# Kernel tuning notes

Hardware: AMD Instinct MI355X
Metric: run time of the kernel (lower is better)

## Reference

```python
import jax, jax.numpy as jnp
import numpy as np

IN, H, B = 1024, 1024, 8192


def _uniform(key, shape, stdv):
    return jax.random.uniform(key, shape, jnp.float32, -stdv, stdv)


def setup_inputs() -> dict:
    key = jax.random.key(0)
    ks = jax.random.split(key, 20)
    stdv = 1.0 / np.sqrt(H)
    inp = {
        "x": jax.random.normal(ks[0], (B, IN), jnp.float32),
        "h": jax.random.normal(ks[1], (B, H), jnp.float32),
        "c": jax.random.normal(ks[2], (B, H), jnp.float32),
        # fused input->gates weight [IN, 4H] (gate order: I, F, G, O) and bias [4H]
        "Wi": _uniform(ks[3], (IN, 4 * H), stdv),
        "bi": _uniform(ks[4], (4 * H,), stdv),
        # fused hidden->gates weight [H, 4H] and bias [4H]
        "Wh": _uniform(ks[5], (H, 4 * H), stdv),
        "bh": _uniform(ks[6], (4 * H,), stdv),
    }
    return inp


def reference(x, h, c, Wi, bi, Wh, bh):
    # Two fused GEMMs replacing the 8 separate nn.Linear calls (same math).
    gates = x @ Wi + bi + h @ Wh + bh  # [B, 4H]
    gI, gF, gG, gO = jnp.split(gates, 4, axis=-1)
    I = jax.nn.sigmoid(gI)
    F = jax.nn.sigmoid(gF)
    G = jnp.tanh(gG)   # nlF = Tanh
    O = jax.nn.sigmoid(gO)
    c_ = F * c + I * G
    h_ = O * jnp.tanh(c_)  # nlF2 = Tanh
    return (h_, c_)
```

## Files before the change

kernel.cpp:

```cpp
#include <hip/hip_runtime.h>
#include <stdint.h>

#define IN_DIM 1024
#define H_DIM  1024
#define BATCH  8192
#define KDIM   2048
#define NDIM   4096
#define BM     256
#define BN     256
#define BK     64
#define NT     (KDIM / BK)

typedef __bf16 bf16x8 __attribute__((ext_vector_type(8)));
typedef float  f32x4  __attribute__((ext_vector_type(4)));
typedef unsigned int u32;

static __device__ __forceinline__ unsigned short f2bf(float f) {
  u32 u = __builtin_bit_cast(u32, f);
  u += 0x7FFFu + ((u >> 16) & 1u);
  return (unsigned short)(u >> 16);
}

static __device__ __forceinline__ float sigm(float x) {
  return 1.0f / (1.0f + __expf(-x));
}
static __device__ __forceinline__ float tanh_fast(float x) {
  float e = __expf(-2.0f * fabsf(x));
  float t = (1.0f - e) / (1.0f + e);
  return copysignf(t, x);
}

__global__ void prep_all(const float* __restrict__ x, const float* __restrict__ h,
                         const float* __restrict__ Wi, const float* __restrict__ Wh,
                         const float* __restrict__ bi, const float* __restrict__ bh,
                         unsigned short* __restrict__ A,
                         unsigned short* __restrict__ Bt,
                         float* __restrict__ bias) {
  __shared__ float tile[32][33];
  const int b = blockIdx.x;
  const int t = threadIdx.x;

  if (b < 2048) {
    const int total = BATCH * KDIM / 4;
    for (int i = b * 256 + t; i < total; i += 2048 * 256) {
      int bb = i >> 9;
      int k = (i & 511) << 2;
      const float* src = (k < IN_DIM) ? (x + (size_t)bb * IN_DIM + k)
                                      : (h + (size_t)bb * H_DIM + (k - IN_DIM));
      float4 v = *reinterpret_cast<const float4*>(src);
      ushort4 o;
      o.x = f2bf(v.x); o.y = f2bf(v.y); o.z = f2bf(v.z); o.w = f2bf(v.w);
      *reinterpret_cast<ushort4*>(A + (size_t)bb * KDIM + k) = o;
    }
  } else if (b < 10240) {
    int bb = b - 2048;
    int k0 = (bb & 63) * 32;
    int c0 = (bb >> 6) * 32;
    int tx = t & 31;
    int ty = t >> 5;
    const float* src = (k0 < IN_DIM) ? (Wi + (size_t)k0 * NDIM)
                                     : (Wh + (size_t)(k0 - IN_DIM) * NDIM);
    for (int i = 0; i < 4; i++) {
      int r = ty + 8 * i;
      tile[r][tx] = src[(size_t)r * NDIM + c0 + tx];
    }
    __syncthreads();
    int g = c0 >> 10;
    int ubase = c0 & 1023;
    for (int i = 0; i < 4; i++) {
      int cc = ty + 8 * i;
      int u = ubase + cc;
      int j = ((u >> 4) << 6) + (g << 4) + (u & 15);
      Bt[(size_t)j * KDIM + k0 + tx] = f2bf(tile[tx][cc]);
    }
  } else {
    int j = (b - 10240) * 256 + t;
    int u = ((j >> 6) << 4) + (j & 15);
    int g = (j >> 4) & 3;
    int c = (g << 10) + u;
    bias[j] = bi[c] + bh[c];
  }
}

static __device__ __forceinline__ void gload_lds16(const void* g, void* l) {
  __builtin_amdgcn_global_load_lds(
      (const __attribute__((address_space(1))) u32*)g,
      (__attribute__((address_space(3))) u32*)l, 16, 0, 0);
}

#define MFMA __builtin_amdgcn_mfma_f32_16x16x32_bf16
#define SGB  __builtin_amdgcn_sched_group_barrier

__launch_bounds__(512, 2)
__global__ void lstm_gemm(const unsigned short* __restrict__ A,
                          const unsigned short* __restrict__ Bt,
                          const float* __restrict__ bias,
                          const float* __restrict__ Cin,
                          float* __restrict__ Hout,
                          float* __restrict__ Cout) {
  __shared__ __align__(16) char smem[131072];

  const int t  = threadIdx.x;
  const int l  = t & 63;
  const int w  = t >> 6;
  const int lane16 = l & 15;
  const int kg = l >> 4;
  const int wr = w >> 2;
  const int wc = w & 3;

  int bid = blockIdx.x;
  int swz = (bid & 7) * 64 + (bid >> 3);
  int brow = (swz >> 4) * BM;
  int bcol = (swz & 15) * BN;

  int slot0 = w * 128 + l, slot1 = slot0 + 64;
  int rih0 = slot0 >> 3, rih1 = slot1 >> 3;
  int c0 = (slot0 & 7) ^ (rih0 & 7), c1 = (slot1 & 7) ^ (rih1 & 7);

  const unsigned short* a0q0 = A + (size_t)(brow + (rih0 >> 6) * 128 + (rih0 & 63)) * KDIM + c0 * 8;
  const unsigned short* a0q1 = A + (size_t)(brow + (rih1 >> 6) * 128 + (rih1 & 63)) * KDIM + c1 * 8;
  const unsigned short* a1q0 = a0q0 + 131072;
  const unsigned short* a1q1 = a0q1 + 131072;
  const unsigned short* b0q0 = Bt + (size_t)(bcol + (rih0 >> 5) * 64 + (rih0 & 31)) * KDIM + c0 * 8;
  const unsigned short* b0q1 = Bt + (size_t)(bcol + (rih1 >> 5) * 64 + (rih1 & 31)) * KDIM + c1 * 8;
  const unsigned short* b1q0 = b0q0 + 65536;
  const unsigned short* b1q1 = b0q1 + 65536;

#define GL(gp, loff) gload_lds16((gp), smem + (loff) + w * 2048 + l * 16)

  const int msk = (lane16 & 7) << 4;
  char* vA0 = smem + wr * 8192 + lane16 * 128 + ((kg * 16) ^ msk);
  char* vA1 = smem + wr * 8192 + lane16 * 128 + ((64 + kg * 16) ^ msk);
  char* vB0 = smem + 65536 + wc * 4096 + lane16 * 128 + ((kg * 16) ^ msk);
  char* vB1 = smem + 65536 + wc * 4096 + lane16 * 128 + ((64 + kg * 16) ^ msk);

  f32x4 acc[8][4];
#pragma unroll
  for (int m = 0; m < 8; m++)
#pragma unroll
    for (int n = 0; n < 4; n++) acc[m][n] = (f32x4){0.f, 0.f, 0.f, 0.f};

  GL(a0q0, 0);                 GL(a0q1, 1024);
  GL(b0q0, 65536);             GL(b0q1, 65536 + 1024);
  GL(a1q0, 16384);             GL(a1q1, 16384 + 1024);
  GL(b1q0, 65536 + 16384);     GL(b1q1, 65536 + 16384 + 1024);
  GL(a0q0 + 64, 32768);        GL(a0q1 + 64, 32768 + 1024);
  GL(b0q0 + 64, 65536 + 32768);GL(b0q1 + 64, 65536 + 32768 + 1024);
  asm volatile("s_waitcnt vmcnt(4)" ::: "memory");
  __builtin_amdgcn_s_barrier();
  __builtin_amdgcn_sched_barrier(0);
  GL(a1q0 + 64, 32768 + 16384); GL(a1q1 + 64, 32768 + 16384 + 1024);

  bf16x8 afrA[4][2], afrB[4][2], bfr[4][2];

#pragma unroll
  for (int mm = 0; mm < 4; mm++) {
    afrA[mm][0] = *(const bf16x8*)(vA0 + mm * 2048);
    afrA[mm][1] = *(const bf16x8*)(vA1 + mm * 2048);
  }
#pragma unroll
  for (int nn = 0; nn < 2; nn++) {
    bfr[nn][0] = *(const bf16x8*)(vB0 + nn * 2048);
    bfr[nn][1] = *(const bf16x8*)(vB1 + nn * 2048);
  }
  a0q0 += 128; a0q1 += 128; a1q0 += 128; a1q1 += 128;
  b0q0 += 128; b0q1 += 128; b1q0 += 64;  b1q1 += 64;

#define BODY(P)                                                              \
  {                                                                          \
    \
    GL(b1q0, 65536 + ((P)^1)*32768 + 16384);                                 \
    GL(b1q1, 65536 + ((P)^1)*32768 + 16384 + 1024);                          \
                           \
    __builtin_amdgcn_s_setprio(1);                                           \
    _Pragma("unroll") for (int nn = 2; nn < 4; nn++) {                       \
      bfr[nn][0] = *(const bf16x8*)(vB0 + (P)*32768 + 16384 + (nn-2)*2048);  \
      bfr[nn][1] = *(const bf16x8*)(vB1 + (P)*32768 + 16384 + (nn-2)*2048);  \
    }                                                                        \
    _Pragma("unroll") for (int mm = 0; mm < 4; mm++)                         \
      _Pragma("unroll") for (int nn = 0; nn < 2; nn++) {                     \
        acc[mm][nn] = MFMA(afrA[mm][0], bfr[nn][0], acc[mm][nn], 0, 0, 0);   \
        acc[mm][nn] = MFMA(afrA[mm][1], bfr[nn][1], acc[mm][nn], 0, 0, 0);   \
      }                                                                      \
    SGB(0x100, 1, 0); SGB(0x8, 4, 0);                                        \
    SGB(0x100, 1, 0); SGB(0x8, 4, 0);                                        \
    SGB(0x100, 1, 0); SGB(0x8, 4, 0);                                        \
    SGB(0x100, 1, 0); SGB(0x8, 4, 0);                                        \
    __builtin_amdgcn_s_setprio(0);                                           \
    __builtin_amdgcn_s_barrier();                                 \
    __builtin_amdgcn_sched_barrier(0);                                       \
         \
    GL(a0q0, (P)*32768);                                                     \
    GL(a0q1, (P)*32768 + 1024);                                              \
                       \
    __builtin_amdgcn_s_setprio(1);                                           \
    _Pragma("unroll") for (int mm = 0; mm < 4; mm++) {                       \
      afrB[mm][0] = *(const bf16x8*)(vA0 + (P)*32768 + 16384 + mm*2048);     \
      afrB[mm][1] = *(const bf16x8*)(vA1 + (P)*32768 + 16384 + mm*2048);     \
    }                                                                        \
    _Pragma("unroll") for (int mm = 0; mm < 4; mm++)                         \
      _Pragma("unroll") for (int nn = 2; nn < 4; nn++) {                     \
        acc[mm][nn] = MFMA(afrA[mm][0], bfr[nn][0], acc[mm][nn], 0, 0, 0);   \
        acc[mm][nn] = MFMA(afrA[mm][1], bfr[nn][1], acc[mm][nn], 0, 0, 0);   \
      }                                                                      \
    SGB(0x100, 2, 0); SGB(0x8, 4, 0);                                        \
    SGB(0x100, 2, 0); SGB(0x8, 4, 0);                                        \
    SGB(0x100, 2, 0); SGB(0x8, 4, 0);                                        \
    SGB(0x100, 2, 0); SGB(0x8, 4, 0);                                        \
    __builtin_amdgcn_s_setprio(0);                                           \
        \
    GL(b0q0, 65536 + (P)*32768);                                             \
    GL(b0q1, 65536 + (P)*32768 + 1024);                                      \
                            \
    __builtin_amdgcn_s_setprio(1);                                           \
    _Pragma("unroll") for (int mm = 0; mm < 4; mm++)                         \
      _Pragma("unroll") for (int nn = 0; nn < 2; nn++) {                     \
        acc[4+mm][nn] = MFMA(afrB[mm][0], bfr[nn][0], acc[4+mm][nn], 0, 0, 0);\
        acc[4+mm][nn] = MFMA(afrB[mm][1], bfr[nn][1], acc[4+mm][nn], 0, 0, 0);\
      }                                                                      \
    __builtin_amdgcn_s_setprio(0);                                           \
    \
    asm volatile("s_waitcnt vmcnt(4)" ::: "memory");                         \
    __builtin_amdgcn_s_barrier();                                 \
    __builtin_amdgcn_sched_barrier(0);                                       \
           \
    GL(a1q0, (P)*32768 + 16384);                                             \
    GL(a1q1, (P)*32768 + 16384 + 1024);                                      \
             \
    __builtin_amdgcn_s_setprio(1);                                           \
    _Pragma("unroll") for (int mm = 0; mm < 4; mm++) {                       \
      afrA[mm][0] = *(const bf16x8*)(vA0 + ((P)^1)*32768 + mm*2048);         \
      afrA[mm][1] = *(const bf16x8*)(vA1 + ((P)^1)*32768 + mm*2048);         \
    }                                                                        \
    _Pragma("unroll") for (int nn = 0; nn < 2; nn++) {                       \
      bfr[nn][0] = *(const bf16x8*)(vB0 + ((P)^1)*32768 + nn*2048);          \
      bfr[nn][1] = *(const bf16x8*)(vB1 + ((P)^1)*32768 + nn*2048);          \
    }                                                                        \
    _Pragma("unroll") for (int mm = 0; mm < 4; mm++)                         \
      _Pragma("unroll") for (int nn = 2; nn < 4; nn++) {                     \
        acc[4+mm][nn] = MFMA(afrB[mm][0], bfr[nn][0], acc[4+mm][nn], 0, 0, 0);\
        acc[4+mm][nn] = MFMA(afrB[mm][1], bfr[nn][1], acc[4+mm][nn], 0, 0, 0);\
      }                                                                      \
    SGB(0x100, 3, 0); SGB(0x8, 4, 0);                                        \
    SGB(0x100, 3, 0); SGB(0x8, 4, 0);                                        \
    SGB(0x100, 3, 0); SGB(0x8, 4, 0);                                        \
    SGB(0x100, 3, 0); SGB(0x8, 4, 0);                                        \
    __builtin_amdgcn_s_setprio(0);                                           \
    a0q0 += 64; a0q1 += 64; a1q0 += 64; a1q1 += 64;                          \
    b0q0 += 64; b0q1 += 64; b1q0 += 64; b1q1 += 64;                          \
  }

  for (int it = 0; it < NT / 2; ++it) {
    BODY(0)
    BODY(1)
  }
#undef BODY
#undef GL

  asm volatile("s_waitcnt vmcnt(0)" ::: "memory");

  const int U = (bcol >> 2) + wc * 16 + lane16;
  const float* cinp = Cin + (size_t)(brow + wr * 128 + kg * 4) * H_DIM + U;
  float cin[32];
#pragma unroll
  for (int m = 0; m < 8; m++)
#pragma unroll
    for (int r = 0; r < 4; r++)
      cin[m * 4 + r] = cinp[(size_t)(m * 16 + r) * H_DIM];
  float bv[4];
#pragma unroll
  for (int nn = 0; nn < 4; nn++)
    bv[nn] = bias[bcol + wc * 64 + nn * 16 + lane16];

  float* hp = Hout + (size_t)(brow + wr * 128 + kg * 4) * H_DIM + U;
  float* cp = Cout + (size_t)(brow + wr * 128 + kg * 4) * H_DIM + U;
#pragma unroll
  for (int m = 0; m < 8; m++)
#pragma unroll
    for (int r = 0; r < 4; r++) {
      float Ig = sigm(acc[m][0][r] + bv[0]);
      float Fg = sigm(acc[m][1][r] + bv[1]);
      float Gg = tanh_fast(acc[m][2][r] + bv[2]);
      float Og = sigm(acc[m][3][r] + bv[3]);
      float cn = Fg * cin[m * 4 + r] + Ig * Gg;
      size_t off = (size_t)(m * 16 + r) * H_DIM;
      hp[off] = Og * tanh_fast(cn);
      cp[off] = cn;
    }
}

extern "C" void kernel_launch(void* const* d_in, const int* in_sizes, int n_in,
                              void* d_out, int out_size, void* d_ws, size_t ws_size,
                              hipStream_t stream) {
  const float* x  = (const float*)d_in[0];
  const float* h  = (const float*)d_in[1];
  const float* c  = (const float*)d_in[2];
  const float* Wi = (const float*)d_in[3];
  const float* bi = (const float*)d_in[4];
  const float* Wh = (const float*)d_in[5];
  const float* bh = (const float*)d_in[6];

  float* out  = (float*)d_out;
  float* Hout = out;
  float* Cout = out + (size_t)BATCH * H_DIM;

  unsigned short* Abf = (unsigned short*)d_ws;
  unsigned short* Btb = (unsigned short*)((char*)d_ws + 33554432);
  float*          bsf = (float*)((char*)d_ws + 50331648);

  prep_all<<<10256, 256, 0, stream>>>(x, h, Wi, Wh, bi, bh, Abf, Btb, bsf);
  lstm_gemm<<<512, 512, 0, stream>>>(Abf, Btb, bsf, c, Hout, Cout);
}
```

Baseline: 152.1 us.

## Shrink GEMM block tile to 128x256 with BK=32 and 4-wave blocks

```diff
diff --git a/kernel.cpp b/kernel.cpp
--- a/kernel.cpp
+++ b/kernel.cpp
@@ -6,9 +6,9 @@
 #define BATCH  8192
 #define KDIM   2048
 #define NDIM   4096
-#define BM     256
+#define BM     128
 #define BN     256
-#define BK     64
+#define BK     32
 #define NT     (KDIM / BK)
 
 typedef __bf16 bf16x8 __attribute__((ext_vector_type(8)));
@@ -91,48 +91,43 @@
 #define MFMA __builtin_amdgcn_mfma_f32_16x16x32_bf16
 #define SGB  __builtin_amdgcn_sched_group_barrier
 
-__launch_bounds__(512, 2)
+__launch_bounds__(256, 2)
 __global__ void lstm_gemm(const unsigned short* __restrict__ A,
                           const unsigned short* __restrict__ Bt,
                           const float* __restrict__ bias,
                           const float* __restrict__ Cin,
                           float* __restrict__ Hout,
                           float* __restrict__ Cout) {
-  __shared__ __align__(16) char smem[131072];
+  __shared__ __align__(16) char smem[49152];
 
   const int t  = threadIdx.x;
   const int l  = t & 63;
   const int w  = t >> 6;
   const int lane16 = l & 15;
   const int kg = l >> 4;
-  const int wr = w >> 2;
-  const int wc = w & 3;
+  const int wc = w;
 
   int bid = blockIdx.x;
-  int swz = (bid & 7) * 64 + (bid >> 3);
-  int brow = (swz >> 4) * BM;
-  int bcol = (swz & 15) * BN;
-
-  int slot0 = w * 128 + l, slot1 = slot0 + 64;
-  int rih0 = slot0 >> 3, rih1 = slot1 >> 3;
-  int c0 = (slot0 & 7) ^ (rih0 & 7), c1 = (slot1 & 7) ^ (rih1 & 7);
-
-  const unsigned short* a0q0 = A + (size_t)(brow + (rih0 >> 6) * 128 + (rih0 & 63)) * KDIM + c0 * 8;
-  const unsigned short* a0q1 = A + (size_t)(brow + (rih1 >> 6) * 128 + (rih1 & 63)) * KDIM + c1 * 8;
-  const unsigned short* a1q0 = a0q0 + 131072;
-  const unsigned short* a1q1 = a0q1 + 131072;
-  const unsigned short* b0q0 = Bt + (size_t)(bcol + (rih0 >> 5) * 64 + (rih0 & 31)) * KDIM + c0 * 8;
-  const unsigned short* b0q1 = Bt + (size_t)(bcol + (rih1 >> 5) * 64 + (rih1 & 31)) * KDIM + c1 * 8;
-  const unsigned short* b1q0 = b0q0 + 65536;
-  const unsigned short* b1q1 = b0q1 + 65536;
-
-#define GL(gp, loff) gload_lds16((gp), smem + (loff) + w * 2048 + l * 16)
-
-  const int msk = (lane16 & 7) << 4;
-  char* vA0 = smem + wr * 8192 + lane16 * 128 + ((kg * 16) ^ msk);
-  char* vA1 = smem + wr * 8192 + lane16 * 128 + ((64 + kg * 16) ^ msk);
-  char* vB0 = smem + 65536 + wc * 4096 + lane16 * 128 + ((kg * 16) ^ msk);
-  char* vB1 = smem + 65536 + wc * 4096 + lane16 * 128 + ((64 + kg * 16) ^ msk);
+  int swz = (bid & 7) * 128 + (bid >> 3);
+  int tile_m = swz >> 4;
+  int tile_n = swz & 15;
+  int brow = tile_m * BM;
+  int bRowB = tile_n * BN;
+
+  const int cth = (l & 3) ^ ((l >> 3) & 3);
+  const int srow = w * 16 + (l >> 2);
+  const unsigned short* aq0 = A + (size_t)(brow + srow) * KDIM + cth * 8;
+  const unsigned short* aq1 = aq0 + (size_t)64 * KDIM;
+  const unsigned short* bq0 = Bt + (size_t)(bRowB + srow) * KDIM + cth * 8;
+  const unsigned short* bq1 = bq0 + (size_t)64 * KDIM;
+  const unsigned short* bq2 = bq0 + (size_t)128 * KDIM;
+  const unsigned short* bq3 = bq0 + (size_t)192 * KDIM;
+
+#define GL(gp, loff) gload_lds16((gp), smem + (loff) + w * 1024 + l * 16)
+
+  const int rsw = ((kg ^ ((lane16 >> 1) & 3)) << 4);
+  char* vRA = smem + lane16 * 64 + rsw;
+  char* vRB = smem + 16384 + wc * 4096 + lane16 * 64 + rsw;
 
   f32x4 acc[8][4];
 #pragma unroll
@@ -140,114 +135,82 @@
 #pragma unroll
     for (int n = 0; n < 4; n++) acc[m][n] = (f32x4){0.f, 0.f, 0.f, 0.f};
 
-  GL(a0q0, 0);                 GL(a0q1, 1024);
-  GL(b0q0, 65536);             GL(b0q1, 65536 + 1024);
-  GL(a1q0, 16384);             GL(a1q1, 16384 + 1024);
-  GL(b1q0, 65536 + 16384);     GL(b1q1, 65536 + 16384 + 1024);
-  GL(a0q0 + 64, 32768);        GL(a0q1 + 64, 32768 + 1024);
-  GL(b0q0 + 64, 65536 + 32768);GL(b0q1 + 64, 65536 + 32768 + 1024);
+  GL(bq0, 16384);          GL(bq1, 16384 + 4096);
+  GL(bq2, 16384 + 8192);   GL(bq3, 16384 + 12288);
+  GL(aq0, 0);              GL(aq1, 4096);
+  GL(bq0 + 32, 32768);         GL(bq1 + 32, 32768 + 4096);
+  GL(bq2 + 32, 32768 + 8192);  GL(bq3 + 32, 32768 + 12288);
   asm volatile("s_waitcnt vmcnt(4)" ::: "memory");
   __builtin_amdgcn_s_barrier();
   __builtin_amdgcn_sched_barrier(0);
-  GL(a1q0 + 64, 32768 + 16384); GL(a1q1 + 64, 32768 + 16384 + 1024);
-
-  bf16x8 afrA[4][2], afrB[4][2], bfr[4][2];
-
-#pragma unroll
-  for (int mm = 0; mm < 4; mm++) {
-    afrA[mm][0] = *(const bf16x8*)(vA0 + mm * 2048);
-    afrA[mm][1] = *(const bf16x8*)(vA1 + mm * 2048);
-  }
-#pragma unroll
-  for (int nn = 0; nn < 2; nn++) {
-    bfr[nn][0] = *(const bf16x8*)(vB0 + nn * 2048);
-    bfr[nn][1] = *(const bf16x8*)(vB1 + nn * 2048);
-  }
-  a0q0 += 128; a0q1 += 128; a1q0 += 128; a1q1 += 128;
-  b0q0 += 128; b0q1 += 128; b1q0 += 64;  b1q1 += 64;
+  GL(aq0 + 32, 8192);      GL(aq1 + 32, 8192 + 4096);
+
+  bf16x8 afrA[4], afrB[4], bfrX[2], bfrY[2];
+#pragma unroll
+  for (int mm = 0; mm < 4; mm++)
+    afrA[mm] = *(const bf16x8*)(vRA + mm * 1024);
+#pragma unroll
+  for (int nn = 0; nn < 2; nn++)
+    bfrX[nn] = *(const bf16x8*)(vRB + nn * 1024);
+  aq0 += 64; aq1 += 64; bq0 += 64; bq1 += 64; bq2 += 64; bq3 += 64;
 
 #define BODY(P)                                                              \
   {                                                                          \
-    \
-    GL(b1q0, 65536 + ((P)^1)*32768 + 16384);                                 \
-    GL(b1q1, 65536 + ((P)^1)*32768 + 16384 + 1024);                          \
-                           \
-    __builtin_amdgcn_s_setprio(1);                                           \
-    _Pragma("unroll") for (int nn = 2; nn < 4; nn++) {                       \
-      bfr[nn][0] = *(const bf16x8*)(vB0 + (P)*32768 + 16384 + (nn-2)*2048);  \
-      bfr[nn][1] = *(const bf16x8*)(vB1 + (P)*32768 + 16384 + (nn-2)*2048);  \
-    }                                                                        \
-    _Pragma("unroll") for (int mm = 0; mm < 4; mm++)                         \
-      _Pragma("unroll") for (int nn = 0; nn < 2; nn++) {                     \
-        acc[mm][nn] = MFMA(afrA[mm][0], bfr[nn][0], acc[mm][nn], 0, 0, 0);   \
-        acc[mm][nn] = MFMA(afrA[mm][1], bfr[nn][1], acc[mm][nn], 0, 0, 0);   \
-      }                                                                      \
+        \
+    __builtin_amdgcn_s_setprio(1);                                           \
+    _Pragma("unroll") for (int nn = 0; nn < 2; nn++)                         \
+      bfrY[nn] = *(const bf16x8*)(vRB + (P)*16384 + (2+nn)*1024);            \
+    _Pragma("unroll") for (int mm = 0; mm < 4; mm++)                         \
+      _Pragma("unroll") for (int nn = 0; nn < 2; nn++)                       \
+        acc[mm][nn] = MFMA(afrA[mm], bfrX[nn], acc[mm][nn], 0, 0, 0);        \
     SGB(0x100, 1, 0); SGB(0x8, 4, 0);                                        \
     SGB(0x100, 1, 0); SGB(0x8, 4, 0);                                        \
-    SGB(0x100, 1, 0); SGB(0x8, 4, 0);                                        \
-    SGB(0x100, 1, 0); SGB(0x8, 4, 0);                                        \
     __builtin_amdgcn_s_setprio(0);                                           \
     __builtin_amdgcn_s_barrier();                                 \
     __builtin_amdgcn_sched_barrier(0);                                       \
-         \
-    GL(a0q0, (P)*32768);                                                     \
-    GL(a0q1, (P)*32768 + 1024);                                              \
-                       \
-    __builtin_amdgcn_s_setprio(1);                                           \
-    _Pragma("unroll") for (int mm = 0; mm < 4; mm++) {                       \
-      afrB[mm][0] = *(const bf16x8*)(vA0 + (P)*32768 + 16384 + mm*2048);     \
-      afrB[mm][1] = *(const bf16x8*)(vA1 + (P)*32768 + 16384 + mm*2048);     \
-    }                                                                        \
-    _Pragma("unroll") for (int mm = 0; mm < 4; mm++)                         \
-      _Pragma("unroll") for (int nn = 2; nn < 4; nn++) {                     \
-        acc[mm][nn] = MFMA(afrA[mm][0], bfr[nn][0], acc[mm][nn], 0, 0, 0);   \
-        acc[mm][nn] = MFMA(afrA[mm][1], bfr[nn][1], acc[mm][nn], 0, 0, 0);   \
-      }                                                                      \
-    SGB(0x100, 2, 0); SGB(0x8, 4, 0);                                        \
-    SGB(0x100, 2, 0); SGB(0x8, 4, 0);                                        \
-    SGB(0x100, 2, 0); SGB(0x8, 4, 0);                                        \
-    SGB(0x100, 2, 0); SGB(0x8, 4, 0);                                        \
-    __builtin_amdgcn_s_setprio(0);                                           \
+                                             \
+    GL(bq0, 16384 + (P)*16384);                                              \
+    GL(bq1, 16384 + (P)*16384 + 4096);                                       \
+    GL(bq2, 16384 + (P)*16384 + 8192);                                       \
+    GL(bq3, 16384 + (P)*16384 + 12288);                                      \
         \
-    GL(b0q0, 65536 + (P)*32768);                                             \
-    GL(b0q1, 65536 + (P)*32768 + 1024);                                      \
-                            \
-    __builtin_amdgcn_s_setprio(1);                                           \
-    _Pragma("unroll") for (int mm = 0; mm < 4; mm++)                         \
-      _Pragma("unroll") for (int nn = 0; nn < 2; nn++) {                     \
-        acc[4+mm][nn] = MFMA(afrB[mm][0], bfr[nn][0], acc[4+mm][nn], 0, 0, 0);\
-        acc[4+mm][nn] = MFMA(afrB[mm][1], bfr[nn][1], acc[4+mm][nn], 0, 0, 0);\
-      }                                                                      \
-    __builtin_amdgcn_s_setprio(0);                                           \
-    \
+    __builtin_amdgcn_s_setprio(1);                                           \
+    _Pragma("unroll") for (int mm = 0; mm < 4; mm++)                         \
+      afrB[mm] = *(const bf16x8*)(vRA + (P)*8192 + (4+mm)*1024);             \
+    _Pragma("unroll") for (int mm = 0; mm < 4; mm++)                         \
+      _Pragma("unroll") for (int nn = 2; nn < 4; nn++)                       \
+        acc[mm][nn] = MFMA(afrA[mm], bfrY[nn-2], acc[mm][nn], 0, 0, 0);      \
+    SGB(0x100, 1, 0); SGB(0x8, 2, 0);                                        \
+    SGB(0x100, 1, 0); SGB(0x8, 2, 0);                                        \
+    SGB(0x100, 1, 0); SGB(0x8, 2, 0);                                        \
+    SGB(0x100, 1, 0); SGB(0x8, 2, 0);                                        \
+    __builtin_amdgcn_s_setprio(0);                                           \
+                  \
+    __builtin_amdgcn_s_setprio(1);                                           \
+    _Pragma("unroll") for (int mm = 0; mm < 4; mm++)                         \
+      _Pragma("unroll") for (int nn = 0; nn < 2; nn++)                       \
+        acc[4+mm][nn] = MFMA(afrB[mm], bfrX[nn], acc[4+mm][nn], 0, 0, 0);    \
+    __builtin_amdgcn_s_setprio(0);                                           \
+                        \
     asm volatile("s_waitcnt vmcnt(4)" ::: "memory");                         \
     __builtin_amdgcn_s_barrier();                                 \
     __builtin_amdgcn_sched_barrier(0);                                       \
-           \
-    GL(a1q0, (P)*32768 + 16384);                                             \
-    GL(a1q1, (P)*32768 + 16384 + 1024);                                      \
-             \
-    __builtin_amdgcn_s_setprio(1);                                           \
-    _Pragma("unroll") for (int mm = 0; mm < 4; mm++) {                       \
-      afrA[mm][0] = *(const bf16x8*)(vA0 + ((P)^1)*32768 + mm*2048);         \
-      afrA[mm][1] = *(const bf16x8*)(vA1 + ((P)^1)*32768 + mm*2048);         \
-    }                                                                        \
-    _Pragma("unroll") for (int nn = 0; nn < 2; nn++) {                       \
-      bfr[nn][0] = *(const bf16x8*)(vB0 + ((P)^1)*32768 + nn*2048);          \
-      bfr[nn][1] = *(const bf16x8*)(vB1 + ((P)^1)*32768 + nn*2048);          \
-    }                                                                        \
-    _Pragma("unroll") for (int mm = 0; mm < 4; mm++)                         \
-      _Pragma("unroll") for (int nn = 2; nn < 4; nn++) {                     \
-        acc[4+mm][nn] = MFMA(afrB[mm][0], bfr[nn][0], acc[4+mm][nn], 0, 0, 0);\
-        acc[4+mm][nn] = MFMA(afrB[mm][1], bfr[nn][1], acc[4+mm][nn], 0, 0, 0);\
-      }                                                                      \
+            \
+    GL(aq0, (P)*8192);                                                       \
+    GL(aq1, (P)*8192 + 4096);                                                \
+          \
+    __builtin_amdgcn_s_setprio(1);                                           \
+    _Pragma("unroll") for (int mm = 0; mm < 4; mm++)                         \
+      afrA[mm] = *(const bf16x8*)(vRA + ((P)^1)*8192 + mm*1024);             \
+    _Pragma("unroll") for (int nn = 0; nn < 2; nn++)                         \
+      bfrX[nn] = *(const bf16x8*)(vRB + ((P)^1)*16384 + nn*1024);            \
+    _Pragma("unroll") for (int mm = 0; mm < 4; mm++)                         \
+      _Pragma("unroll") for (int nn = 2; nn < 4; nn++)                       \
+        acc[4+mm][nn] = MFMA(afrB[mm], bfrY[nn-2], acc[4+mm][nn], 0, 0, 0);  \
     SGB(0x100, 3, 0); SGB(0x8, 4, 0);                                        \
     SGB(0x100, 3, 0); SGB(0x8, 4, 0);                                        \
-    SGB(0x100, 3, 0); SGB(0x8, 4, 0);                                        \
-    SGB(0x100, 3, 0); SGB(0x8, 4, 0);                                        \
-    __builtin_amdgcn_s_setprio(0);                                           \
-    a0q0 += 64; a0q1 += 64; a1q0 += 64; a1q1 += 64;                          \
-    b0q0 += 64; b0q1 += 64; b1q0 += 64; b1q1 += 64;                          \
+    __builtin_amdgcn_s_setprio(0);                                           \
+    aq0 += 32; aq1 += 32; bq0 += 32; bq1 += 32; bq2 += 32; bq3 += 32;        \
   }
 
   for (int it = 0; it < NT / 2; ++it) {
@@ -259,8 +222,8 @@
 
   asm volatile("s_waitcnt vmcnt(0)" ::: "memory");
 
-  const int U = (bcol >> 2) + wc * 16 + lane16;
-  const float* cinp = Cin + (size_t)(brow + wr * 128 + kg * 4) * H_DIM + U;
+  const int U = tile_n * 64 + wc * 16 + lane16;
+  const float* cinp = Cin + (size_t)(brow + kg * 4) * H_DIM + U;
   float cin[32];
 #pragma unroll
   for (int m = 0; m < 8; m++)
@@ -270,10 +233,10 @@
   float bv[4];
 #pragma unroll
   for (int nn = 0; nn < 4; nn++)
-    bv[nn] = bias[bcol + wc * 64 + nn * 16 + lane16];
-
-  float* hp = Hout + (size_t)(brow + wr * 128 + kg * 4) * H_DIM + U;
-  float* cp = Cout + (size_t)(brow + wr * 128 + kg * 4) * H_DIM + U;
+    bv[nn] = bias[tile_n * 256 + wc * 64 + nn * 16 + lane16];
+
+  float* hp = Hout + (size_t)(brow + kg * 4) * H_DIM + U;
+  float* cp = Cout + (size_t)(brow + kg * 4) * H_DIM + U;
 #pragma unroll
   for (int m = 0; m < 8; m++)
 #pragma unroll
@@ -309,5 +272,5 @@
   float*          bsf = (float*)((char*)d_ws + 50331648);
 
   prep_all<<<10256, 256, 0, stream>>>(x, h, Wi, Wh, bi, bh, Abf, Btb, bsf);
-  lstm_gemm<<<512, 512, 0, stream>>>(Abf, Btb, bsf, c, Hout, Cout);
-}
+  lstm_gemm<<<1024, 256, 0, stream>>>(Abf, Btb, bsf, c, Hout, Cout);
+}
```

Result: slower. 172.6 us (+13.5%).
